# Optimization experiments

Hardware: AMD Instinct MI355X
Metric: run time of the kernel (lower is better)

Reference implementation:

```python
import jax, jax.numpy as jnp
import numpy as np

B, N, D, H, A = 1024, 16, 64, 64, 64
TAU = 0.01   # gumbel-softmax temperature from the source
EPS = 1e-10


def setup_inputs() -> dict:
    key = jax.random.key(0)
    ks = jax.random.split(key, 23)

    def rn(k, shape, s=0.05):
        return jax.random.normal(k, shape, dtype=jnp.float32) * s

    return {
        "obs": jax.random.normal(ks[0], (B, N, D), dtype=jnp.float32),
        "hidden_state": jax.random.normal(ks[1], (B * N, A), dtype=jnp.float32),
        "gumbel_u": jax.random.uniform(ks[2], (B * N * (N - 1), 2), dtype=jnp.float32,
                                       minval=1e-6, maxval=1.0 - 1e-6),
        "W_enc": rn(ks[3], (D, H)), "b_enc": rn(ks[4], (H,)),
        "Wih_f": rn(ks[5], (3 * H, 2 * H)), "Whh_f": rn(ks[6], (3 * H, H)),
        "bih_f": rn(ks[7], (3 * H,)), "bhh_f": rn(ks[8], (3 * H,)),
        "Wih_b": rn(ks[9], (3 * H, 2 * H)), "Whh_b": rn(ks[10], (3 * H, H)),
        "bih_b": rn(ks[11], (3 * H,)), "bhh_b": rn(ks[12], (3 * H,)),
        "W_hard": rn(ks[13], (2 * H, 2)), "b_hard": rn(ks[14], (2,)),
        "Wq": rn(ks[15], (H, A)), "Wk": rn(ks[16], (H, A)),
        "Wv": rn(ks[17], (H, A)), "b_v": rn(ks[18], (A,)),
        "Wih_c": rn(ks[19], (3 * A, A)), "Whh_c": rn(ks[20], (3 * A, A)),
        "bih_c": rn(ks[21], (3 * A,)), "bhh_c": rn(ks[22], (3 * A,)),
    }


def _gru_scan(x_seq, Wih, Whh, bih, bhh):
    # x_seq: [T, BN, 2H]; PyTorch GRU gate order r, z, n. Input projection
    # for all timesteps is precomputed (one big GEMM) outside the scan.
    gi = jnp.einsum('tbd,gd->tbg', x_seq, Wih) + bih  # [T, BN, 3H]
    h0 = jnp.zeros((x_seq.shape[1], Whh.shape[1]), x_seq.dtype)

    def step(h, gi_t):
        gh = h @ Whh.T + bhh
        i_r, i_z, i_n = jnp.split(gi_t, 3, axis=-1)
        h_r, h_z, h_n = jnp.split(gh, 3, axis=-1)
        r = jax.nn.sigmoid(i_r + h_r)
        z = jax.nn.sigmoid(i_z + h_z)
        n = jnp.tanh(i_n + r * h_n)
        h_new = (1.0 - z) * n + z * h
        return h_new, h_new

    _, out = jax.lax.scan(step, h0, gi)
    return out  # [T, BN, H]


def _gru_cell(x, h, Wih, Whh, bih, bhh):
    gi = x @ Wih.T + bih
    gh = h @ Whh.T + bhh
    i_r, i_z, i_n = jnp.split(gi, 3, axis=-1)
    h_r, h_z, h_n = jnp.split(gh, 3, axis=-1)
    r = jax.nn.sigmoid(i_r + h_r)
    z = jax.nn.sigmoid(i_z + h_z)
    n = jnp.tanh(i_n + r * h_n)
    return (1.0 - z) * n + z * h


def reference(obs, hidden_state, gumbel_u, W_enc, b_enc,
              Wih_f, Whh_f, bih_f, bhh_f, Wih_b, Whh_b, bih_b, bhh_b,
              W_hard, b_hard, Wq, Wk, Wv, b_v,
              Wih_c, Whh_c, bih_c, bhh_c):
    b, n, d = obs.shape
    h_enc = jax.nn.relu(obs @ W_enc + b_enc)          # [B, N, H]
    h_flat = h_enc.reshape(-1, H)                      # [B*N, H]

    # static neighbor index table: row i lists all j != i
    j_idx = np.array([[j for j in range(n) if j != i] for i in range(n)])  # [N, N-1]

    # pairwise concat features, vectorized (replaces the double python loop)
    h_j = h_enc[:, j_idx]                               # [B, N, N-1, H]
    h_i = jnp.broadcast_to(h_enc[:, :, None, :], h_j.shape)
    pair = jnp.concatenate([h_i, h_j], axis=-1)        # [B, N, N-1, 2H]
    input_hard = pair.transpose(2, 0, 1, 3).reshape(n - 1, b * n, 2 * H)

    # bidirectional GRU over the N-1 neighbor axis
    out_f = _gru_scan(input_hard, Wih_f, Whh_f, bih_f, bhh_f)
    out_b = _gru_scan(input_hard[::-1], Wih_b, Whh_b, bih_b, bhh_b)[::-1]
    h_hard = jnp.concatenate([out_f, out_b], axis=-1)  # [N-1, B*N, 2H]
    h_hard = h_hard.transpose(1, 0, 2).reshape(-1, 2 * H)

    # hard gate: gumbel-softmax (soft sample, tau=0.01), take channel 1
    logits = h_hard @ W_hard + b_hard                   # [B*N*(N-1), 2]
    g = -jnp.log(-jnp.log(gumbel_u + EPS) + EPS)
    hard = jax.nn.softmax((logits + g) / TAU, axis=-1)
    hard_w = hard[:, 1].reshape(b, n, n - 1)            # [B, N, N-1]

    # scaled dot-product attention over neighbors j != i
    q = (h_flat @ Wq).reshape(b, n, A)
    k = (h_flat @ Wk).reshape(b, n, A)
    v = jax.nn.relu(h_flat @ Wv + b_v).reshape(b, n, A)
    k_j = k[:, j_idx]                                   # [B, N, N-1, A]
    v_j = v[:, j_idx]
    score = jnp.einsum('bna,bnja->bnj', q, k_j) / float(np.sqrt(A))
    soft = jax.nn.softmax(score, axis=-1)
    x = jnp.einsum('bnja,bnj->bna', v_j, soft * hard_w).reshape(b * n, A)

    return _gru_cell(x, hidden_state, Wih_c, Whh_c, bih_c, bhh_c)
```

## Files before the change

### kernel.cpp

```cpp
#include <hip/hip_runtime.h>
#include <hip/hip_bf16.h>
#include <stdint.h>

#define NNODE 16384
#define TAU_ 0.01f
#define EPSG 1e-10f

#define OFF_WENC 0
#define OFF_BENC 4096
#define OFF_WIHF_H 4160
#define OFF_WIHF_L 16448
#define OFF_WHHF_H 28736
#define OFF_BIHF 41024
#define OFF_BHHF 41216
#define OFF_WIHB_H 41408
#define OFF_WIHB_L 53696
#define OFF_WHHB_H 65984
#define OFF_BIHB 78272
#define OFF_BHHB 78464
#define OFF_WHARD 78656
#define OFF_BHARD 78912
#define OFF_WQT_H 78914
#define OFF_WQT_L 80962
#define OFF_WKT_H 83010
#define OFF_WKT_L 85058
#define OFF_WVT_H 87106
#define OFF_WVT_L 89154
#define OFF_BV 91202
#define OFF_WIHC_H 91266
#define OFF_WIHC_L 97410
#define OFF_WHHC_H 103554
#define OFF_WHHC_L 109698
#define OFF_BIHC 115842
#define OFF_BHHC 116034
#define OFF_WENCT_H 118784
#define OFF_WENCT_L 120832
#define OFF_YF 131072
#define OFF_YB (OFF_YF + 491520)
#define WS_FLOATS (OFF_YB + 491520)

typedef float  v4f __attribute__((ext_vector_type(4)));
typedef short  v8s __attribute__((ext_vector_type(8)));

__device__ __forceinline__ float rcpf(float x){ return __builtin_amdgcn_rcpf(x); }
__device__ __forceinline__ float sigf(float x){ return rcpf(1.0f + __expf(-x)); }
__device__ __forceinline__ float tanhfast(float x){ return 1.0f - 2.0f*rcpf(__expf(2.0f*x)+1.0f); }
__device__ __forceinline__ unsigned short f2bf(float f){
  __hip_bfloat16 h = __float2bfloat16(f);
  return *reinterpret_cast<unsigned short*>(&h);
}
__device__ __forceinline__ float bf2f(unsigned short u){
  union { unsigned int i; float f; } v; v.i = ((unsigned int)u) << 16; return v.f;
}

struct Prep {
  const float* s[20];
  int n[20];
  int o[20];
};
__global__ void k_prep(Prep p, float* __restrict__ ws){
  int a = blockIdx.y;
  int i = blockIdx.x * blockDim.x + threadIdx.x;
  if (i < p.n[a]) ws[p.o[a] + i] = p.s[a][i];
}

__global__ void k_prep2(const float* __restrict__ wenc,
                        const float* __restrict__ wihf, const float* __restrict__ wihb,
                        const float* __restrict__ whhf, const float* __restrict__ whhb,
                        const float* __restrict__ wq,   const float* __restrict__ wk,
                        const float* __restrict__ wv,   const float* __restrict__ wihc,
                        const float* __restrict__ whhc,
                        float* __restrict__ ws){
  int a = blockIdx.y;
  int i = blockIdx.x * blockDim.x + threadIdx.x;
  if (a == 0 || (a >= 5 && a <= 7)){
    if (i < 4096){
      const float* src = (a==0) ? wenc : (a==5) ? wq : (a==6) ? wk : wv;
      int oh = (a==0) ? OFF_WENCT_H : (a==5) ? OFF_WQT_H : (a==6) ? OFF_WKT_H : OFF_WVT_H;
      int ol = (a==0) ? OFF_WENCT_L : oh + 2048;
      float x = src[((i & 63) << 6) | (i >> 6)];
      unsigned short h = f2bf(x);
      unsigned short l = f2bf(x - bf2f(h));
      ((unsigned short*)(ws + oh))[i] = h;
      ((unsigned short*)(ws + ol))[i] = l;
    }
  } else if (a == 1 || a == 2){
    if (i < 24576){
      float x = (a == 1 ? wihf : wihb)[i];
      unsigned short h = f2bf(x);
      unsigned short l = f2bf(x - bf2f(h));
      ((unsigned short*)(ws + (a == 1 ? OFF_WIHF_H : OFF_WIHB_H)))[i] = h;
      ((unsigned short*)(ws + (a == 1 ? OFF_WIHF_L : OFF_WIHB_L)))[i] = l;
    }
  } else if (a == 3 || a == 4){
    if (i < 12288){
      float x = (a == 3 ? whhf : whhb)[i];
      ((unsigned short*)(ws + (a == 3 ? OFF_WHHF_H : OFF_WHHB_H)))[i] = f2bf(x);
    }
  } else {
    if (i < 12288){
      float x = (a == 8 ? wihc : whhc)[i];
      unsigned short h = f2bf(x);
      unsigned short l = f2bf(x - bf2f(h));
      int oh = (a == 8 ? OFF_WIHC_H : OFF_WHHC_H);
      ((unsigned short*)(ws + oh))[i] = h;
      ((unsigned short*)(ws + oh + 6144))[i] = l;
    }
  }
}

__global__ __launch_bounds__(256, 2) void k_gru(const float* __restrict__ obs,
                                                float* __restrict__ ws){
  __shared__ float smem[9216];
  float* s_u2 = smem;
  unsigned short* s_obs_h = (unsigned short*)(smem + 6272);
  unsigned short* s_obs_l = s_obs_h + 2304;
  unsigned short* s_hbu   = (unsigned short*)(smem + 6272);
  float* s_red = smem + 9088;

  const int tid = threadIdx.x;
  const int nl  = tid & 63;
  const int grp = __builtin_amdgcn_readfirstlane(tid >> 6);
  const int dir = blockIdx.x >> 9;
  const int base = (blockIdx.x & 511) * 32;
  const int lw = grp >> 1;
  const int nw = grp & 1;
  const int q  = nl >> 4;
  const int i_c = nl & 15;
  const int node = 16*nw + i_c;

  {
    float4 a = *(const float4*)&obs[base*64 + tid*8];
    float4 b = *(const float4*)&obs[base*64 + tid*8 + 4];
    int nn = tid >> 3, d0 = (tid & 7)*8;
    union { v8s v; unsigned short u[8]; } H, L;
    float xs[8] = {a.x,a.y,a.z,a.w,b.x,b.y,b.z,b.w};
    #pragma unroll
    for (int e = 0; e < 8; e++){
      H.u[e] = f2bf(xs[e]);
      L.u[e] = f2bf(xs[e] - bf2f(H.u[e]));
    }
    *(v8s*)&s_obs_h[nn*72 + d0] = H.v;
    *(v8s*)&s_obs_l[nn*72 + d0] = L.v;
  }
  __syncthreads();

  const float* benc = ws + OFF_BENC;
  const unsigned short* wtH = (const unsigned short*)(ws + OFF_WENCT_H);
  const unsigned short* wtL = (const unsigned short*)(ws + OFF_WENCT_L);
  v4f dEnc[2];
  {
    v8s obH[2], obL[2];
    #pragma unroll
    for (int kc = 0; kc < 2; kc++){
      int ba = node*72 + kc*32 + q*8;
      obH[kc] = *(const v8s*)&s_obs_h[ba];
      obL[kc] = *(const v8s*)&s_obs_l[ba];
    }
    #pragma unroll
    for (int tt = 0; tt < 2; tt++){
      int lT = 2*lw + tt;
      float4 bi = *(const float4*)&benc[16*lT + 4*q];
      v4f d = (v4f){bi.x, bi.y, bi.z, bi.w};
      #pragma unroll
      for (int kc = 0; kc < 2; kc++){
        int aa = (16*lT + i_c)*64 + kc*32 + q*8;
        v8s aH = *(const v8s*)&wtH[aa];
        v8s aL = *(const v8s*)&wtL[aa];
        d = __builtin_amdgcn_mfma_f32_16x16x32_bf16(aH, obH[kc], d, 0,0,0);
        d = __builtin_amdgcn_mfma_f32_16x16x32_bf16(aH, obL[kc], d, 0,0,0);
        d = __builtin_amdgcn_mfma_f32_16x16x32_bf16(aL, obH[kc], d, 0,0,0);
      }
      dEnc[tt] = d;
    }
  }
  __syncthreads();
  #pragma unroll
  for (int tt = 0; tt < 2; tt++){
    int lT = 2*lw + tt;
    unsigned short hh[4], ll[4];
    #pragma unroll
    for (int r = 0; r < 4; r++){
      float v = fmaxf(dEnc[tt][r], 0.0f);
      hh[r] = f2bf(v);
      ll[r] = f2bf(v - bf2f(hh[r]));
    }
    int wa = node*72 + 16*lT + 4*q;
    *(uint2*)&s_obs_h[wa] = make_uint2((unsigned)hh[0] | ((unsigned)hh[1]<<16),
                                       (unsigned)hh[2] | ((unsigned)hh[3]<<16));
    *(uint2*)&s_obs_l[wa] = make_uint2((unsigned)ll[0] | ((unsigned)ll[1]<<16),
                                       (unsigned)ll[2] | ((unsigned)ll[3]<<16));
  }
  __syncthreads();

  const float* bih = ws + (dir ? OFF_BIHB : OFF_BIHF);
  const float* bhh = ws + (dir ? OFF_BHHB : OFF_BHHF);
  const unsigned short* wiH = (const unsigned short*)(ws + (dir ? OFF_WIHB_H : OFF_WIHF_H));
  const unsigned short* wiL = (const unsigned short*)(ws + (dir ? OFF_WIHB_L : OFF_WIHF_L));
  const unsigned short* whH = (const unsigned short*)(ws + (dir ? OFF_WHHB_H : OFF_WHHF_H));

  v8s hbH[2], hbL[2];
  #pragma unroll
  for (int kc = 0; kc < 2; kc++){
    int ba = node*72 + kc*32 + q*8;
    hbH[kc] = *(const v8s*)&s_obs_h[ba];
    hbL[kc] = *(const v8s*)&s_obs_l[ba];
  }

  #pragma unroll
  for (int m = 0; m < 6; m++){
    int T = 6*lw + m;
    v4f d = (v4f){0.f,0.f,0.f,0.f};
    #pragma unroll
    for (int kc = 0; kc < 2; kc++){
      int aa = (16*T + i_c)*128 + 64 + kc*32 + q*8;
      v8s aH = *(const v8s*)&wiH[aa];
      v8s aL = *(const v8s*)&wiL[aa];
      d = __builtin_amdgcn_mfma_f32_16x16x32_bf16(aH, hbH[kc], d, 0,0,0);
      d = __builtin_amdgcn_mfma_f32_16x16x32_bf16(aH, hbL[kc], d, 0,0,0);
      d = __builtin_amdgcn_mfma_f32_16x16x32_bf16(aL, hbH[kc], d, 0,0,0);
    }
    *(v4f*)&s_u2[node*196 + 16*T + 4*q] = d;
  }

  v4f cbr[2], cbz[2], cbn[2], bhn4[2];
  #pragma unroll
  for (int g = 0; g < 3; g++){
    #pragma unroll
    for (int t2 = 0; t2 < 2; t2++){
      int row0 = 64*g + 32*lw + 16*t2 + 4*q;
      float4 bi = *(const float4*)&bih[row0];
      v4f d;
      if (g < 2){
        float4 bh = *(const float4*)&bhh[row0];
        d = (v4f){bi.x+bh.x, bi.y+bh.y, bi.z+bh.z, bi.w+bh.w};
      } else {
        d = (v4f){bi.x, bi.y, bi.z, bi.w};
      }
      int T = (64*g + 32*lw + 16*t2) >> 4;
      #pragma unroll
      for (int kc = 0; kc < 2; kc++){
        int aa = (16*T + i_c)*128 + kc*32 + q*8;
        v8s aH = *(const v8s*)&wiH[aa];
        v8s aL = *(const v8s*)&wiL[aa];
        d = __builtin_amdgcn_mfma_f32_16x16x32_bf16(aH, hbH[kc], d, 0,0,0);
        d = __builtin_amdgcn_mfma_f32_16x16x32_bf16(aH, hbL[kc], d, 0,0,0);
        d = __builtin_amdgcn_mfma_f32_16x16x32_bf16(aL, hbH[kc], d, 0,0,0);
      }
      if (g == 0) cbr[t2] = d; else if (g == 1) cbz[t2] = d; else cbn[t2] = d;
    }
  }
  #pragma unroll
  for (int t2 = 0; t2 < 2; t2++){
    int row0 = 128 + 32*lw + 16*t2 + 4*q;
    float4 nh = *(const float4*)&bhh[row0];
    bhn4[t2] = (v4f){nh.x, nh.y, nh.z, nh.w};
  }

  v8s afr[2][2], afz[2][2], afn[2][2];
  #pragma unroll
  for (int t2 = 0; t2 < 2; t2++){
    #pragma unroll
    for (int kc = 0; kc < 2; kc++){
      #pragma unroll
      for (int g = 0; g < 3; g++){
        int row = g*64 + 32*lw + 16*t2 + i_c;
        v8s a = *(const v8s*)&whH[row*64 + kc*32 + q*8];
        if (g == 0) afr[t2][kc] = a; else if (g == 1) afz[t2][kc] = a; else afn[t2][kc] = a;
      }
    }
  }

  const float* whard = ws + OFF_WHARD + dir*128;
  float wh0[8], wh1[8];
  #pragma unroll
  for (int t2 = 0; t2 < 2; t2++){
    #pragma unroll
    for (int r = 0; r < 4; r++){
      int l = 32*lw + 16*t2 + 4*q + r;
      wh0[t2*4+r] = whard[l*2];
      wh1[t2*4+r] = whard[l*2+1];
    }
  }
  __syncthreads();

  float* yout = ws + (dir ? OFF_YB : OFF_YF);

  float hv[8];
  #pragma unroll
  for (int m = 0; m < 8; m++) hv[m] = 0.0f;

  for (int kk = 0; kk < 15; kk++){
    const int t  = dir ? (14 - kk) : kk;
    const int j  = t + (t >= i_c ? 1 : 0);
    const int jl = 16*nw + j;
    const int rb = kk & 1;
    const int wb = (kk + 1) & 1;

    v8s b0, b1;
    if (kk > 0){
      const unsigned short* rp = s_hbu + rb*2816 + node*88 + q*8;
      b0 = *(const v8s*)(rp);
      b1 = *(const v8s*)(rp + 32);
    }

    float a0p = 0.f, a1p = 0.f;
    #pragma unroll
    for (int t2 = 0; t2 < 2; t2++){
      int l0 = 32*lw + 16*t2 + 4*q;
      v4f dr = cbr[t2], dz = cbz[t2];
      v4f dn = (v4f){0.f,0.f,0.f,0.f};
      if (kk > 0){
        dr = __builtin_amdgcn_mfma_f32_16x16x32_bf16(afr[t2][0], b0, dr, 0,0,0);
        dr = __builtin_amdgcn_mfma_f32_16x16x32_bf16(afr[t2][1], b1, dr, 0,0,0);
        dz = __builtin_amdgcn_mfma_f32_16x16x32_bf16(afz[t2][0], b0, dz, 0,0,0);
        dz = __builtin_amdgcn_mfma_f32_16x16x32_bf16(afz[t2][1], b1, dz, 0,0,0);
        dn = __builtin_amdgcn_mfma_f32_16x16x32_bf16(afn[t2][0], b0, dn, 0,0,0);
        dn = __builtin_amdgcn_mfma_f32_16x16x32_bf16(afn[t2][1], b1, dn, 0,0,0);
      }
      v4f ur = *(const v4f*)&s_u2[jl*196 +       l0];
      v4f uz = *(const v4f*)&s_u2[jl*196 +  64 + l0];
      v4f un = *(const v4f*)&s_u2[jl*196 + 128 + l0];
      float hn[4];
      #pragma unroll
      for (int r = 0; r < 4; r++){
        float rg = sigf(dr[r] + ur[r]);
        float zg = sigf(dz[r] + uz[r]);
        float ng = tanhfast(cbn[t2][r] + un[r] + rg*(bhn4[t2][r] + dn[r]));
        float hnew = (1.0f - zg)*ng + zg*hv[t2*4+r];
        hv[t2*4+r] = hnew;
        hn[r] = hnew;
        a0p += hnew*wh0[t2*4+r];
        a1p += hnew*wh1[t2*4+r];
      }
      unsigned int p0 = (unsigned int)f2bf(hn[0]) | ((unsigned int)f2bf(hn[1]) << 16);
      unsigned int p1 = (unsigned int)f2bf(hn[2]) | ((unsigned int)f2bf(hn[3]) << 16);
      *(uint2*)(s_hbu + wb*2816 + node*88 + l0) = make_uint2(p0, p1);
    }

    a0p += __shfl_xor(a0p, 16); a0p += __shfl_xor(a0p, 32);
    a1p += __shfl_xor(a1p, 16); a1p += __shfl_xor(a1p, 32);
    float* sr = s_red + rb*64;
    if (lw == 0 && q == 0)
      *(float2*)&sr[node*2] = make_float2(a0p, a1p);
    __syncthreads();
    if (lw == 1 && q == 0){
      float2 pp = *(const float2*)&sr[node*2];
      *(float2*)&yout[((base + node)*15 + t)*2] = make_float2(a0p + pp.x, a1p + pp.y);
    }
  }
}

__global__ __launch_bounds__(256, 1) void k_attn(const float* __restrict__ obs,
                                                 const float* __restrict__ hid,
                                                 const float* __restrict__ gum,
                                                 float* __restrict__ ws,
                                                 float* __restrict__ out){
  __shared__ float smem[7200];
  unsigned short* s_obs_h = (unsigned short*)smem;
  unsigned short* s_obs_l = s_obs_h + 2304;
  float* s_q  = smem;
  unsigned short* s_h0h = (unsigned short*)smem;
  unsigned short* s_h0l = s_h0h + 2304;
  float* s_k  = smem + 2304;
  unsigned short* s_xh = (unsigned short*)(smem + 2304);
  unsigned short* s_xl = s_xh + 2304;
  float* s_v  = smem + 4608;
  float* s_co = smem + 6720;

  const int tid = threadIdx.x;
  const int nl  = tid & 63;
  const int grp = __builtin_amdgcn_readfirstlane(tid >> 6);
  const int base = blockIdx.x * 32;
  const int lw = grp >> 1;
  const int nw = grp & 1;
  const int q4 = nl >> 4;
  const int i_c = nl & 15;
  const int node = 16*nw + i_c;

  {
    float4 a = *(const float4*)&obs[base*64 + tid*8];
    float4 b = *(const float4*)&obs[base*64 + tid*8 + 4];
    int nn = tid >> 3, d0 = (tid & 7)*8;
    union { v8s v; unsigned short u[8]; } H, L;
    float xs[8] = {a.x,a.y,a.z,a.w,b.x,b.y,b.z,b.w};
    #pragma unroll
    for (int e = 0; e < 8; e++){
      H.u[e] = f2bf(xs[e]);
      L.u[e] = f2bf(xs[e] - bf2f(H.u[e]));
    }
    *(v8s*)&s_obs_h[nn*72 + d0] = H.v;
    *(v8s*)&s_obs_l[nn*72 + d0] = L.v;
  }
  __syncthreads();

  const float* benc = ws + OFF_BENC;
  const unsigned short* wtH = (const unsigned short*)(ws + OFF_WENCT_H);
  const unsigned short* wtL = (const unsigned short*)(ws + OFF_WENCT_L);
  v4f dEnc[2];
  {
    v8s obH[2], obL[2];
    #pragma unroll
    for (int kc = 0; kc < 2; kc++){
      int ba = node*72 + kc*32 + q4*8;
      obH[kc] = *(const v8s*)&s_obs_h[ba];
      obL[kc] = *(const v8s*)&s_obs_l[ba];
    }
    #pragma unroll
    for (int tt = 0; tt < 2; tt++){
      int lT = 2*lw + tt;
      float4 bi = *(const float4*)&benc[16*lT + 4*q4];
      v4f d = (v4f){bi.x, bi.y, bi.z, bi.w};
      #pragma unroll
      for (int kc = 0; kc < 2; kc++){
        int aa = (16*lT + i_c)*64 + kc*32 + q4*8;
        v8s aH = *(const v8s*)&wtH[aa];
        v8s aL = *(const v8s*)&wtL[aa];
        d = __builtin_amdgcn_mfma_f32_16x16x32_bf16(aH, obH[kc], d, 0,0,0);
        d = __builtin_amdgcn_mfma_f32_16x16x32_bf16(aH, obL[kc], d, 0,0,0);
        d = __builtin_amdgcn_mfma_f32_16x16x32_bf16(aL, obH[kc], d, 0,0,0);
      }
      dEnc[tt] = d;
    }
  }
  __syncthreads();
  #pragma unroll
  for (int tt = 0; tt < 2; tt++){
    int lT = 2*lw + tt;
    unsigned short hh[4], ll[4];
    #pragma unroll
    for (int r = 0; r < 4; r++){
      float v = fmaxf(dEnc[tt][r], 0.0f);
      hh[r] = f2bf(v);
      ll[r] = f2bf(v - bf2f(hh[r]));
    }
    int wa = node*72 + 16*lT + 4*q4;
    *(uint2*)&s_obs_h[wa] = make_uint2((unsigned)hh[0] | ((unsigned)hh[1]<<16),
                                       (unsigned)hh[2] | ((unsigned)hh[3]<<16));
    *(uint2*)&s_obs_l[wa] = make_uint2((unsigned)ll[0] | ((unsigned)ll[1]<<16),
                                       (unsigned)ll[2] | ((unsigned)ll[3]<<16));
  }
  __syncthreads();

  v8s hbH[2], hbL[2];
  #pragma unroll
  for (int kc = 0; kc < 2; kc++){
    int ba = node*72 + kc*32 + q4*8;
    hbH[kc] = *(const v8s*)&s_obs_h[ba];
    hbL[kc] = *(const v8s*)&s_obs_l[ba];
  }
  const unsigned short* wqH = (const unsigned short*)(ws + OFF_WQT_H);
  const unsigned short* wqL = (const unsigned short*)(ws + OFF_WQT_L);
  const unsigned short* wkH = (const unsigned short*)(ws + OFF_WKT_H);
  const unsigned short* wkL = (const unsigned short*)(ws + OFF_WKT_L);
  const unsigned short* wvH = (const unsigned short*)(ws + OFF_WVT_H);
  const unsigned short* wvL = (const unsigned short*)(ws + OFF_WVT_L);
  const float* bv = ws + OFF_BV;
  v4f dq[2], dk[2], dv[2];
  #pragma unroll
  for (int a2 = 0; a2 < 2; a2++){
    int aT = 2*lw + a2;
    v4f q_ = (v4f){0.f,0.f,0.f,0.f};
    v4f k_ = (v4f){0.f,0.f,0.f,0.f};
    float4 b4 = *(const float4*)&bv[16*aT + 4*q4];
    v4f v_ = (v4f){b4.x, b4.y, b4.z, b4.w};
    #pragma unroll
    for (int kc = 0; kc < 2; kc++){
      int ai = (16*aT + i_c)*64 + kc*32 + q4*8;
      v8s aH = *(const v8s*)&wqH[ai]; v8s aL = *(const v8s*)&wqL[ai];
      q_ = __builtin_amdgcn_mfma_f32_16x16x32_bf16(aH, hbH[kc], q_, 0,0,0);
      q_ = __builtin_amdgcn_mfma_f32_16x16x32_bf16(aH, hbL[kc], q_, 0,0,0);
      q_ = __builtin_amdgcn_mfma_f32_16x16x32_bf16(aL, hbH[kc], q_, 0,0,0);
      aH = *(const v8s*)&wkH[ai]; aL = *(const v8s*)&wkL[ai];
      k_ = __builtin_amdgcn_mfma_f32_16x16x32_bf16(aH, hbH[kc], k_, 0,0,0);
      k_ = __builtin_amdgcn_mfma_f32_16x16x32_bf16(aH, hbL[kc], k_, 0,0,0);
      k_ = __builtin_amdgcn_mfma_f32_16x16x32_bf16(aL, hbH[kc], k_, 0,0,0);
      aH = *(const v8s*)&wvH[ai]; aL = *(const v8s*)&wvL[ai];
      v_ = __builtin_amdgcn_mfma_f32_16x16x32_bf16(aH, hbH[kc], v_, 0,0,0);
      v_ = __builtin_amdgcn_mfma_f32_16x16x32_bf16(aH, hbL[kc], v_, 0,0,0);
      v_ = __builtin_amdgcn_mfma_f32_16x16x32_bf16(aL, hbH[kc], v_, 0,0,0);
    }
    dq[a2] = q_; dk[a2] = k_; dv[a2] = v_;
  }
  __syncthreads();

  #pragma unroll
  for (int a2 = 0; a2 < 2; a2++){
    int aT = 2*lw + a2;
    *(v4f*)&s_q[node*68 + 16*aT + 4*q4] = dq[a2];
    #pragma unroll
    for (int r = 0; r < 4; r++){
      s_k[(16*aT + 4*q4 + r)*33 + node] = dk[a2][r];
      s_v[(16*aT + 4*q4 + r)*33 + node] = fmaxf(dv[a2][r], 0.f);
    }
  }
  __syncthreads();

  const int n2  = tid >> 3;
  const int asl = tid & 7;
  const int ib2 = n2 & 15, jb2 = n2 & 16;
  float4 aq0 = *(const float4*)&s_q[n2*68 + asl*8];
  float4 aq1 = *(const float4*)&s_q[n2*68 + asl*8 + 4];
  float sc[15];
  #pragma unroll
  for (int t = 0; t < 15; t++){
    int jl = jb2 | (t + (t >= ib2 ? 1 : 0));
    const float* kp = s_k + (asl*8)*33 + jl;
    float s = aq0.x*kp[0]  + aq0.y*kp[33]  + aq0.z*kp[66]  + aq0.w*kp[99]
            + aq1.x*kp[132] + aq1.y*kp[165] + aq1.z*kp[198] + aq1.w*kp[231];
    s += __shfl_xor(s, 1); s += __shfl_xor(s, 2); s += __shfl_xor(s, 4);
    sc[t] = s * 0.125f;
  }
  {
    float m = sc[0];
    #pragma unroll
    for (int t = 1; t < 15; t++) m = fmaxf(m, sc[t]);
    float den = 0.f;
    #pragma unroll
    for (int t = 0; t < 15; t++) den += __expf(sc[t]-m);
    float rden = rcpf(den);
    const float bh0 = ws[OFF_BHARD], bh1 = ws[OFF_BHARD+1];
    const float* yF = ws + OFF_YF; const float* yB = ws + OFF_YB;
    #pragma unroll
    for (int t = 0; t < 15; t++){
      if ((t & 7) == asl){
        int rowb = ((base + n2)*15 + t)*2;
        float y0 = yF[rowb]   + yB[rowb]   + bh0;
        float y1 = yF[rowb+1] + yB[rowb+1] + bh1;
        float2 u2 = *(const float2*)&gum[rowb];
        float g0 = -__logf(-__logf(u2.x + EPSG) + EPSG);
        float g1 = -__logf(-__logf(u2.y + EPSG) + EPSG);
        float w  = sigf(((y1+g1) - (y0+g0)) * (1.0f/TAU_));
        s_co[t*32 + n2] = __expf(sc[t]-m)*rden*w;
      }
    }
  }
  __syncthreads();

  {
    float xa[8];
    #pragma unroll
    for (int il = 0; il < 8; il++) xa[il] = 0.f;
    #pragma unroll
    for (int t = 0; t < 15; t++){
      float c = s_co[t*32 + n2];
      int jl = jb2 | (t + (t >= ib2 ? 1 : 0));
      const float* vp = s_v + (asl*8)*33 + jl;
      xa[0] += c*vp[0];    xa[1] += c*vp[33];   xa[2] += c*vp[66];   xa[3] += c*vp[99];
      xa[4] += c*vp[132];  xa[5] += c*vp[165];  xa[6] += c*vp[198];  xa[7] += c*vp[231];
    }
    union { v8s v; unsigned short u[8]; } XH, XL;
    #pragma unroll
    for (int e = 0; e < 8; e++){
      XH.u[e] = f2bf(xa[e]);
      XL.u[e] = f2bf(xa[e] - bf2f(XH.u[e]));
    }
    *(v8s*)&s_xh[n2*72 + asl*8] = XH.v;
    *(v8s*)&s_xl[n2*72 + asl*8] = XL.v;
  }
  {
    float4 a = *(const float4*)&hid[base*64 + tid*8];
    float4 b = *(const float4*)&hid[base*64 + tid*8 + 4];
    int nn = tid >> 3, d0 = (tid & 7)*8;
    union { v8s v; unsigned short u[8]; } H, L;
    float xs[8] = {a.x,a.y,a.z,a.w,b.x,b.y,b.z,b.w};
    #pragma unroll
    for (int e = 0; e < 8; e++){
      H.u[e] = f2bf(xs[e]);
      L.u[e] = f2bf(xs[e] - bf2f(H.u[e]));
    }
    *(v8s*)&s_h0h[nn*72 + d0] = H.v;
    *(v8s*)&s_h0l[nn*72 + d0] = L.v;
  }
  __syncthreads();

  v8s xbH[2], xbL[2], h0H[2], h0L[2];
  #pragma unroll
  for (int kc = 0; kc < 2; kc++){
    int ba = node*72 + kc*32 + q4*8;
    xbH[kc] = *(const v8s*)&s_xh[ba];  xbL[kc] = *(const v8s*)&s_xl[ba];
    h0H[kc] = *(const v8s*)&s_h0h[ba]; h0L[kc] = *(const v8s*)&s_h0l[ba];
  }
  const unsigned short* wiH = (const unsigned short*)(ws + OFF_WIHC_H);
  const unsigned short* wiL = (const unsigned short*)(ws + OFF_WIHC_L);
  const unsigned short* whH = (const unsigned short*)(ws + OFF_WHHC_H);
  const unsigned short* whL = (const unsigned short*)(ws + OFF_WHHC_L);
  const float* bihc = ws + OFF_BIHC; const float* bhhc = ws + OFF_BHHC;
  v4f gi[3][2], gh[3][2];
  #pragma unroll
  for (int g = 0; g < 3; g++){
    #pragma unroll
    for (int u2 = 0; u2 < 2; u2++){
      int u = 2*lw + u2;
      int row0 = g*64 + 16*u + 4*q4;
      float4 bi = *(const float4*)&bihc[row0];
      float4 bh = *(const float4*)&bhhc[row0];
      v4f di, dh;
      if (g < 2){
        di = (v4f){bi.x+bh.x, bi.y+bh.y, bi.z+bh.z, bi.w+bh.w};
        dh = (v4f){0.f,0.f,0.f,0.f};
      } else {
        di = (v4f){bi.x, bi.y, bi.z, bi.w};
        dh = (v4f){bh.x, bh.y, bh.z, bh.w};
      }
      #pragma unroll
      for (int kc = 0; kc < 2; kc++){
        int ai = (g*64 + 16*u + i_c)*64 + kc*32 + q4*8;
        v8s aH = *(const v8s*)&wiH[ai]; v8s aL = *(const v8s*)&wiL[ai];
        di = __builtin_amdgcn_mfma_f32_16x16x32_bf16(aH, xbH[kc], di, 0,0,0);
        di = __builtin_amdgcn_mfma_f32_16x16x32_bf16(aH, xbL[kc], di, 0,0,0);
        di = __builtin_amdgcn_mfma_f32_16x16x32_bf16(aL, xbH[kc], di, 0,0,0);
        aH = *(const v8s*)&whH[ai]; aL = *(const v8s*)&whL[ai];
        dh = __builtin_amdgcn_mfma_f32_16x16x32_bf16(aH, h0H[kc], dh, 0,0,0);
        dh = __builtin_amdgcn_mfma_f32_16x16x32_bf16(aH, h0L[kc], dh, 0,0,0);
        dh = __builtin_amdgcn_mfma_f32_16x16x32_bf16(aL, h0H[kc], dh, 0,0,0);
      }
      gi[g][u2] = di; gh[g][u2] = dh;
    }
  }
  #pragma unroll
  for (int u2 = 0; u2 < 2; u2++){
    int l0 = 16*(2*lw + u2) + 4*q4;
    float4 h04 = *(const float4*)&hid[(base+node)*64 + l0];
    float hh[4] = {h04.x, h04.y, h04.z, h04.w};
    float ho[4];
    #pragma unroll
    for (int r = 0; r < 4; r++){
      float rg = sigf(gi[0][u2][r] + gh[0][u2][r]);
      float zg = sigf(gi[1][u2][r] + gh[1][u2][r]);
      float ng = tanhfast(gi[2][u2][r] + rg*gh[2][u2][r]);
      ho[r] = (1.0f - zg)*ng + zg*hh[r];
    }
    *(float4*)&out[(base+node)*64 + l0] = make_float4(ho[0], ho[1], ho[2], ho[3]);
  }
}

extern "C" void kernel_launch(void* const* d_in, const int* in_sizes, int n_in,
                              void* d_out, int out_size, void* d_ws, size_t ws_size,
                              hipStream_t stream){
  if (ws_size < (size_t)WS_FLOATS * sizeof(float)) return;
  float* ws = (float*)d_ws;
  static const int offs[20] = {OFF_WENC, OFF_BENC, 0, 0, OFF_BIHF, OFF_BHHF,
      0, 0, OFF_BIHB, OFF_BHHB, OFF_WHARD, OFF_BHARD, 0, 0, 0,
      OFF_BV, 0, 0, OFF_BIHC, OFF_BHHC};
  Prep p;
  for (int i = 0; i < 20; i++){
    p.s[i] = (const float*)d_in[3 + i];
    p.n[i] = in_sizes[3 + i];
    p.o[i] = offs[i];
  }
  p.n[2] = 0; p.n[3] = 0; p.n[6] = 0; p.n[7] = 0;
  p.n[12] = 0; p.n[13] = 0; p.n[14] = 0;
  p.n[16] = 0; p.n[17] = 0;
  hipLaunchKernelGGL(k_prep, dim3(96, 20), dim3(256), 0, stream, p, ws);
  hipLaunchKernelGGL(k_prep2, dim3(96, 10), dim3(256), 0, stream,
                     (const float*)d_in[3], (const float*)d_in[5], (const float*)d_in[9],
                     (const float*)d_in[6], (const float*)d_in[10],
                     (const float*)d_in[15], (const float*)d_in[16], (const float*)d_in[17],
                     (const float*)d_in[19], (const float*)d_in[20], ws);
  hipLaunchKernelGGL(k_gru,  dim3(1024),   dim3(256), 0, stream,
                     (const float*)d_in[0], ws);
  hipLaunchKernelGGL(k_attn, dim3(512),    dim3(256), 0, stream,
                     (const float*)d_in[0], (const float*)d_in[1],
                     (const float*)d_in[2], ws, (float*)d_out);
}
```

Before: 187.8 us.

## Fuse bidirectional GRU and attention kernels into one 512-thread block

Merges the separate GRU kernel and attention/output kernel into a single kernel with 512 threads per block, where both directions of the GRU run in the same block (waves split by direction). The encoder is computed once per block instead of three times, and the hard-gate logits stay in shared memory rather than going through a global workspace round-trip. This trades a larger shared-memory footprint and bigger blocks (possibly lower occupancy) and leaves half the threads idle during the attention phase.

```diff
diff --git a/kernel.cpp b/kernel.cpp
--- a/kernel.cpp
+++ b/kernel.cpp
@@ -109,83 +109,88 @@
   }
 }
 
-__global__ __launch_bounds__(256, 2) void k_gru(const float* __restrict__ obs,
-                                                float* __restrict__ ws){
-  __shared__ float smem[9216];
+__global__ __launch_bounds__(512, 2) void k_main(const float* __restrict__ obs,
+                                                 const float* __restrict__ hid,
+                                                 const float* __restrict__ gum,
+                                                 float* __restrict__ ws,
+                                                 float* __restrict__ out){
+  __shared__ float smem[20352];
   float* s_u2 = smem;
-  unsigned short* s_obs_h = (unsigned short*)(smem + 6272);
-  unsigned short* s_obs_l = s_obs_h + 2304;
-  unsigned short* s_hbu   = (unsigned short*)(smem + 6272);
-  float* s_red = smem + 9088;
+  unsigned short* s_B = (unsigned short*)(smem + 12544);
+  unsigned short* s_obs_h = s_B;
+  unsigned short* s_obs_l = s_B + 2304;
+  float* s_red = smem + 18176;
+  float* s_y   = smem + 18432;
+  float* s_q  = smem;
+  float* s_k  = smem + 2176;
+  float* s_v  = smem + 4288;
+  float* s_co = smem + 6400;
 
   const int tid = threadIdx.x;
   const int nl  = tid & 63;
   const int grp = __builtin_amdgcn_readfirstlane(tid >> 6);
-  const int dir = blockIdx.x >> 9;
-  const int base = (blockIdx.x & 511) * 32;
-  const int lw = grp >> 1;
-  const int nw = grp & 1;
-  const int q  = nl >> 4;
+  const int dir = grp >> 2;
+  const int sub = grp & 3;
+  const int lw  = sub >> 1;
+  const int nw  = grp & 1;
+  const int hi2 = grp >> 1;
+  const int q4  = nl >> 4;
   const int i_c = nl & 15;
   const int node = 16*nw + i_c;
-
-  {
-    float4 a = *(const float4*)&obs[base*64 + tid*8];
-    float4 b = *(const float4*)&obs[base*64 + tid*8 + 4];
-    int nn = tid >> 3, d0 = (tid & 7)*8;
-    union { v8s v; unsigned short u[8]; } H, L;
-    float xs[8] = {a.x,a.y,a.z,a.w,b.x,b.y,b.z,b.w};
-    #pragma unroll
-    for (int e = 0; e < 8; e++){
-      H.u[e] = f2bf(xs[e]);
-      L.u[e] = f2bf(xs[e] - bf2f(H.u[e]));
-    }
-    *(v8s*)&s_obs_h[nn*72 + d0] = H.v;
-    *(v8s*)&s_obs_l[nn*72 + d0] = L.v;
+  const int base = blockIdx.x * 32;
+
+  {
+    float4 a = *(const float4*)&obs[base*64 + tid*4];
+    int nn = tid >> 4, d0 = (tid & 15)*4;
+    unsigned short hh[4], ll[4];
+    float xs[4] = {a.x,a.y,a.z,a.w};
+    #pragma unroll
+    for (int e = 0; e < 4; e++){
+      hh[e] = f2bf(xs[e]);
+      ll[e] = f2bf(xs[e] - bf2f(hh[e]));
+    }
+    *(uint2*)&s_obs_h[nn*72 + d0] = make_uint2((unsigned)hh[0] | ((unsigned)hh[1]<<16),
+                                               (unsigned)hh[2] | ((unsigned)hh[3]<<16));
+    *(uint2*)&s_obs_l[nn*72 + d0] = make_uint2((unsigned)ll[0] | ((unsigned)ll[1]<<16),
+                                               (unsigned)ll[2] | ((unsigned)ll[3]<<16));
   }
   __syncthreads();
 
   const float* benc = ws + OFF_BENC;
   const unsigned short* wtH = (const unsigned short*)(ws + OFF_WENCT_H);
   const unsigned short* wtL = (const unsigned short*)(ws + OFF_WENCT_L);
-  v4f dEnc[2];
+  v4f dEnc;
   {
     v8s obH[2], obL[2];
     #pragma unroll
     for (int kc = 0; kc < 2; kc++){
-      int ba = node*72 + kc*32 + q*8;
+      int ba = node*72 + kc*32 + q4*8;
       obH[kc] = *(const v8s*)&s_obs_h[ba];
       obL[kc] = *(const v8s*)&s_obs_l[ba];
     }
-    #pragma unroll
-    for (int tt = 0; tt < 2; tt++){
-      int lT = 2*lw + tt;
-      float4 bi = *(const float4*)&benc[16*lT + 4*q];
-      v4f d = (v4f){bi.x, bi.y, bi.z, bi.w};
-      #pragma unroll
-      for (int kc = 0; kc < 2; kc++){
-        int aa = (16*lT + i_c)*64 + kc*32 + q*8;
-        v8s aH = *(const v8s*)&wtH[aa];
-        v8s aL = *(const v8s*)&wtL[aa];
-        d = __builtin_amdgcn_mfma_f32_16x16x32_bf16(aH, obH[kc], d, 0,0,0);
-        d = __builtin_amdgcn_mfma_f32_16x16x32_bf16(aH, obL[kc], d, 0,0,0);
-        d = __builtin_amdgcn_mfma_f32_16x16x32_bf16(aL, obH[kc], d, 0,0,0);
-      }
-      dEnc[tt] = d;
-    }
-  }
-  __syncthreads();
-  #pragma unroll
-  for (int tt = 0; tt < 2; tt++){
-    int lT = 2*lw + tt;
+    float4 bi = *(const float4*)&benc[16*hi2 + 4*q4];
+    v4f d = (v4f){bi.x, bi.y, bi.z, bi.w};
+    #pragma unroll
+    for (int kc = 0; kc < 2; kc++){
+      int aa = (16*hi2 + i_c)*64 + kc*32 + q4*8;
+      v8s aH = *(const v8s*)&wtH[aa];
+      v8s aL = *(const v8s*)&wtL[aa];
+      d = __builtin_amdgcn_mfma_f32_16x16x32_bf16(aH, obH[kc], d, 0,0,0);
+      d = __builtin_amdgcn_mfma_f32_16x16x32_bf16(aH, obL[kc], d, 0,0,0);
+      d = __builtin_amdgcn_mfma_f32_16x16x32_bf16(aL, obH[kc], d, 0,0,0);
+    }
+    dEnc = d;
+  }
+  __syncthreads();
+  {
     unsigned short hh[4], ll[4];
     #pragma unroll
     for (int r = 0; r < 4; r++){
-      float v = fmaxf(dEnc[tt][r], 0.0f);
+      float v = fmaxf(dEnc[r], 0.0f);
       hh[r] = f2bf(v);
       ll[r] = f2bf(v - bf2f(hh[r]));
     }
-    int wa = node*72 + 16*lT + 4*q;
+    int wa = node*72 + 16*hi2 + 4*q4;
     *(uint2*)&s_obs_h[wa] = make_uint2((unsigned)hh[0] | ((unsigned)hh[1]<<16),
                                        (unsigned)hh[2] | ((unsigned)hh[3]<<16));
     *(uint2*)&s_obs_l[wa] = make_uint2((unsigned)ll[0] | ((unsigned)ll[1]<<16),
@@ -193,255 +198,6 @@
   }
   __syncthreads();
 
-  const float* bih = ws + (dir ? OFF_BIHB : OFF_BIHF);
-  const float* bhh = ws + (dir ? OFF_BHHB : OFF_BHHF);
-  const unsigned short* wiH = (const unsigned short*)(ws + (dir ? OFF_WIHB_H : OFF_WIHF_H));
-  const unsigned short* wiL = (const unsigned short*)(ws + (dir ? OFF_WIHB_L : OFF_WIHF_L));
-  const unsigned short* whH = (const unsigned short*)(ws + (dir ? OFF_WHHB_H : OFF_WHHF_H));
-
-  v8s hbH[2], hbL[2];
-  #pragma unroll
-  for (int kc = 0; kc < 2; kc++){
-    int ba = node*72 + kc*32 + q*8;
-    hbH[kc] = *(const v8s*)&s_obs_h[ba];
-    hbL[kc] = *(const v8s*)&s_obs_l[ba];
-  }
-
-  #pragma unroll
-  for (int m = 0; m < 6; m++){
-    int T = 6*lw + m;
-    v4f d = (v4f){0.f,0.f,0.f,0.f};
-    #pragma unroll
-    for (int kc = 0; kc < 2; kc++){
-      int aa = (16*T + i_c)*128 + 64 + kc*32 + q*8;
-      v8s aH = *(const v8s*)&wiH[aa];
-      v8s aL = *(const v8s*)&wiL[aa];
-      d = __builtin_amdgcn_mfma_f32_16x16x32_bf16(aH, hbH[kc], d, 0,0,0);
-      d = __builtin_amdgcn_mfma_f32_16x16x32_bf16(aH, hbL[kc], d, 0,0,0);
-      d = __builtin_amdgcn_mfma_f32_16x16x32_bf16(aL, hbH[kc], d, 0,0,0);
-    }
-    *(v4f*)&s_u2[node*196 + 16*T + 4*q] = d;
-  }
-
-  v4f cbr[2], cbz[2], cbn[2], bhn4[2];
-  #pragma unroll
-  for (int g = 0; g < 3; g++){
-    #pragma unroll
-    for (int t2 = 0; t2 < 2; t2++){
-      int row0 = 64*g + 32*lw + 16*t2 + 4*q;
-      float4 bi = *(const float4*)&bih[row0];
-      v4f d;
-      if (g < 2){
-        float4 bh = *(const float4*)&bhh[row0];
-        d = (v4f){bi.x+bh.x, bi.y+bh.y, bi.z+bh.z, bi.w+bh.w};
-      } else {
-        d = (v4f){bi.x, bi.y, bi.z, bi.w};
-      }
-      int T = (64*g + 32*lw + 16*t2) >> 4;
-      #pragma unroll
-      for (int kc = 0; kc < 2; kc++){
-        int aa = (16*T + i_c)*128 + kc*32 + q*8;
-        v8s aH = *(const v8s*)&wiH[aa];
-        v8s aL = *(const v8s*)&wiL[aa];
-        d = __builtin_amdgcn_mfma_f32_16x16x32_bf16(aH, hbH[kc], d, 0,0,0);
-        d = __builtin_amdgcn_mfma_f32_16x16x32_bf16(aH, hbL[kc], d, 0,0,0);
-        d = __builtin_amdgcn_mfma_f32_16x16x32_bf16(aL, hbH[kc], d, 0,0,0);
-      }
-      if (g == 0) cbr[t2] = d; else if (g == 1) cbz[t2] = d; else cbn[t2] = d;
-    }
-  }
-  #pragma unroll
-  for (int t2 = 0; t2 < 2; t2++){
-    int row0 = 128 + 32*lw + 16*t2 + 4*q;
-    float4 nh = *(const float4*)&bhh[row0];
-    bhn4[t2] = (v4f){nh.x, nh.y, nh.z, nh.w};
-  }
-
-  v8s afr[2][2], afz[2][2], afn[2][2];
-  #pragma unroll
-  for (int t2 = 0; t2 < 2; t2++){
-    #pragma unroll
-    for (int kc = 0; kc < 2; kc++){
-      #pragma unroll
-      for (int g = 0; g < 3; g++){
-        int row = g*64 + 32*lw + 16*t2 + i_c;
-        v8s a = *(const v8s*)&whH[row*64 + kc*32 + q*8];
-        if (g == 0) afr[t2][kc] = a; else if (g == 1) afz[t2][kc] = a; else afn[t2][kc] = a;
-      }
-    }
-  }
-
-  const float* whard = ws + OFF_WHARD + dir*128;
-  float wh0[8], wh1[8];
-  #pragma unroll
-  for (int t2 = 0; t2 < 2; t2++){
-    #pragma unroll
-    for (int r = 0; r < 4; r++){
-      int l = 32*lw + 16*t2 + 4*q + r;
-      wh0[t2*4+r] = whard[l*2];
-      wh1[t2*4+r] = whard[l*2+1];
-    }
-  }
-  __syncthreads();
-
-  float* yout = ws + (dir ? OFF_YB : OFF_YF);
-
-  float hv[8];
-  #pragma unroll
-  for (int m = 0; m < 8; m++) hv[m] = 0.0f;
-
-  for (int kk = 0; kk < 15; kk++){
-    const int t  = dir ? (14 - kk) : kk;
-    const int j  = t + (t >= i_c ? 1 : 0);
-    const int jl = 16*nw + j;
-    const int rb = kk & 1;
-    const int wb = (kk + 1) & 1;
-
-    v8s b0, b1;
-    if (kk > 0){
-      const unsigned short* rp = s_hbu + rb*2816 + node*88 + q*8;
-      b0 = *(const v8s*)(rp);
-      b1 = *(const v8s*)(rp + 32);
-    }
-
-    float a0p = 0.f, a1p = 0.f;
-    #pragma unroll
-    for (int t2 = 0; t2 < 2; t2++){
-      int l0 = 32*lw + 16*t2 + 4*q;
-      v4f dr = cbr[t2], dz = cbz[t2];
-      v4f dn = (v4f){0.f,0.f,0.f,0.f};
-      if (kk > 0){
-        dr = __builtin_amdgcn_mfma_f32_16x16x32_bf16(afr[t2][0], b0, dr, 0,0,0);
-        dr = __builtin_amdgcn_mfma_f32_16x16x32_bf16(afr[t2][1], b1, dr, 0,0,0);
-        dz = __builtin_amdgcn_mfma_f32_16x16x32_bf16(afz[t2][0], b0, dz, 0,0,0);
-        dz = __builtin_amdgcn_mfma_f32_16x16x32_bf16(afz[t2][1], b1, dz, 0,0,0);
-        dn = __builtin_amdgcn_mfma_f32_16x16x32_bf16(afn[t2][0], b0, dn, 0,0,0);
-        dn = __builtin_amdgcn_mfma_f32_16x16x32_bf16(afn[t2][1], b1, dn, 0,0,0);
-      }
-      v4f ur = *(const v4f*)&s_u2[jl*196 +       l0];
-      v4f uz = *(const v4f*)&s_u2[jl*196 +  64 + l0];
-      v4f un = *(const v4f*)&s_u2[jl*196 + 128 + l0];
-      float hn[4];
-      #pragma unroll
-      for (int r = 0; r < 4; r++){
-        float rg = sigf(dr[r] + ur[r]);
-        float zg = sigf(dz[r] + uz[r]);
-        float ng = tanhfast(cbn[t2][r] + un[r] + rg*(bhn4[t2][r] + dn[r]));
-        float hnew = (1.0f - zg)*ng + zg*hv[t2*4+r];
-        hv[t2*4+r] = hnew;
-        hn[r] = hnew;
-        a0p += hnew*wh0[t2*4+r];
-        a1p += hnew*wh1[t2*4+r];
-      }
-      unsigned int p0 = (unsigned int)f2bf(hn[0]) | ((unsigned int)f2bf(hn[1]) << 16);
-      unsigned int p1 = (unsigned int)f2bf(hn[2]) | ((unsigned int)f2bf(hn[3]) << 16);
-      *(uint2*)(s_hbu + wb*2816 + node*88 + l0) = make_uint2(p0, p1);
-    }
-
-    a0p += __shfl_xor(a0p, 16); a0p += __shfl_xor(a0p, 32);
-    a1p += __shfl_xor(a1p, 16); a1p += __shfl_xor(a1p, 32);
-    float* sr = s_red + rb*64;
-    if (lw == 0 && q == 0)
-      *(float2*)&sr[node*2] = make_float2(a0p, a1p);
-    __syncthreads();
-    if (lw == 1 && q == 0){
-      float2 pp = *(const float2*)&sr[node*2];
-      *(float2*)&yout[((base + node)*15 + t)*2] = make_float2(a0p + pp.x, a1p + pp.y);
-    }
-  }
-}
-
-__global__ __launch_bounds__(256, 1) void k_attn(const float* __restrict__ obs,
-                                                 const float* __restrict__ hid,
-                                                 const float* __restrict__ gum,
-                                                 float* __restrict__ ws,
-                                                 float* __restrict__ out){
-  __shared__ float smem[7200];
-  unsigned short* s_obs_h = (unsigned short*)smem;
-  unsigned short* s_obs_l = s_obs_h + 2304;
-  float* s_q  = smem;
-  unsigned short* s_h0h = (unsigned short*)smem;
-  unsigned short* s_h0l = s_h0h + 2304;
-  float* s_k  = smem + 2304;
-  unsigned short* s_xh = (unsigned short*)(smem + 2304);
-  unsigned short* s_xl = s_xh + 2304;
-  float* s_v  = smem + 4608;
-  float* s_co = smem + 6720;
-
-  const int tid = threadIdx.x;
-  const int nl  = tid & 63;
-  const int grp = __builtin_amdgcn_readfirstlane(tid >> 6);
-  const int base = blockIdx.x * 32;
-  const int lw = grp >> 1;
-  const int nw = grp & 1;
-  const int q4 = nl >> 4;
-  const int i_c = nl & 15;
-  const int node = 16*nw + i_c;
-
-  {
-    float4 a = *(const float4*)&obs[base*64 + tid*8];
-    float4 b = *(const float4*)&obs[base*64 + tid*8 + 4];
-    int nn = tid >> 3, d0 = (tid & 7)*8;
-    union { v8s v; unsigned short u[8]; } H, L;
-    float xs[8] = {a.x,a.y,a.z,a.w,b.x,b.y,b.z,b.w};
-    #pragma unroll
-    for (int e = 0; e < 8; e++){
-      H.u[e] = f2bf(xs[e]);
-      L.u[e] = f2bf(xs[e] - bf2f(H.u[e]));
-    }
-    *(v8s*)&s_obs_h[nn*72 + d0] = H.v;
-    *(v8s*)&s_obs_l[nn*72 + d0] = L.v;
-  }
-  __syncthreads();
-
-  const float* benc = ws + OFF_BENC;
-  const unsigned short* wtH = (const unsigned short*)(ws + OFF_WENCT_H);
-  const unsigned short* wtL = (const unsigned short*)(ws + OFF_WENCT_L);
-  v4f dEnc[2];
-  {
-    v8s obH[2], obL[2];
-    #pragma unroll
-    for (int kc = 0; kc < 2; kc++){
-      int ba = node*72 + kc*32 + q4*8;
-      obH[kc] = *(const v8s*)&s_obs_h[ba];
-      obL[kc] = *(const v8s*)&s_obs_l[ba];
-    }
-    #pragma unroll
-    for (int tt = 0; tt < 2; tt++){
-      int lT = 2*lw + tt;
-      float4 bi = *(const float4*)&benc[16*lT + 4*q4];
-      v4f d = (v4f){bi.x, bi.y, bi.z, bi.w};
-      #pragma unroll
-      for (int kc = 0; kc < 2; kc++){
-        int aa = (16*lT + i_c)*64 + kc*32 + q4*8;
-        v8s aH = *(const v8s*)&wtH[aa];
-        v8s aL = *(const v8s*)&wtL[aa];
-        d = __builtin_amdgcn_mfma_f32_16x16x32_bf16(aH, obH[kc], d, 0,0,0);
-        d = __builtin_amdgcn_mfma_f32_16x16x32_bf16(aH, obL[kc], d, 0,0,0);
-        d = __builtin_amdgcn_mfma_f32_16x16x32_bf16(aL, obH[kc], d, 0,0,0);
-      }
-      dEnc[tt] = d;
-    }
-  }
-  __syncthreads();
-  #pragma unroll
-  for (int tt = 0; tt < 2; tt++){
-    int lT = 2*lw + tt;
-    unsigned short hh[4], ll[4];
-    #pragma unroll
-    for (int r = 0; r < 4; r++){
-      float v = fmaxf(dEnc[tt][r], 0.0f);
-      hh[r] = f2bf(v);
-      ll[r] = f2bf(v - bf2f(hh[r]));
-    }
-    int wa = node*72 + 16*lT + 4*q4;
-    *(uint2*)&s_obs_h[wa] = make_uint2((unsigned)hh[0] | ((unsigned)hh[1]<<16),
-                                       (unsigned)hh[2] | ((unsigned)hh[3]<<16));
-    *(uint2*)&s_obs_l[wa] = make_uint2((unsigned)ll[0] | ((unsigned)ll[1]<<16),
-                                       (unsigned)ll[2] | ((unsigned)ll[3]<<16));
-  }
-  __syncthreads();
-
   v8s hbH[2], hbL[2];
   #pragma unroll
   for (int kc = 0; kc < 2; kc++){
@@ -449,24 +205,23 @@
     hbH[kc] = *(const v8s*)&s_obs_h[ba];
     hbL[kc] = *(const v8s*)&s_obs_l[ba];
   }
-  const unsigned short* wqH = (const unsigned short*)(ws + OFF_WQT_H);
-  const unsigned short* wqL = (const unsigned short*)(ws + OFF_WQT_L);
-  const unsigned short* wkH = (const unsigned short*)(ws + OFF_WKT_H);
-  const unsigned short* wkL = (const unsigned short*)(ws + OFF_WKT_L);
-  const unsigned short* wvH = (const unsigned short*)(ws + OFF_WVT_H);
-  const unsigned short* wvL = (const unsigned short*)(ws + OFF_WVT_L);
-  const float* bv = ws + OFF_BV;
-  v4f dq[2], dk[2], dv[2];
-  #pragma unroll
-  for (int a2 = 0; a2 < 2; a2++){
-    int aT = 2*lw + a2;
+
+  v4f dq, dk, dv;
+  {
+    const unsigned short* wqH = (const unsigned short*)(ws + OFF_WQT_H);
+    const unsigned short* wqL = (const unsigned short*)(ws + OFF_WQT_L);
+    const unsigned short* wkH = (const unsigned short*)(ws + OFF_WKT_H);
+    const unsigned short* wkL = (const unsigned short*)(ws + OFF_WKT_L);
+    const unsigned short* wvH = (const unsigned short*)(ws + OFF_WVT_H);
+    const unsigned short* wvL = (const unsigned short*)(ws + OFF_WVT_L);
+    const float* bv = ws + OFF_BV;
     v4f q_ = (v4f){0.f,0.f,0.f,0.f};
     v4f k_ = (v4f){0.f,0.f,0.f,0.f};
-    float4 b4 = *(const float4*)&bv[16*aT + 4*q4];
+    float4 b4 = *(const float4*)&bv[16*hi2 + 4*q4];
     v4f v_ = (v4f){b4.x, b4.y, b4.z, b4.w};
     #pragma unroll
     for (int kc = 0; kc < 2; kc++){
-      int ai = (16*aT + i_c)*64 + kc*32 + q4*8;
+      int ai = (16*hi2 + i_c)*64 + kc*32 + q4*8;
       v8s aH = *(const v8s*)&wqH[ai]; v8s aL = *(const v8s*)&wqL[ai];
       q_ = __builtin_amdgcn_mfma_f32_16x16x32_bf16(aH, hbH[kc], q_, 0,0,0);
       q_ = __builtin_amdgcn_mfma_f32_16x16x32_bf16(aH, hbL[kc], q_, 0,0,0);
@@ -480,18 +235,165 @@
       v_ = __builtin_amdgcn_mfma_f32_16x16x32_bf16(aH, hbL[kc], v_, 0,0,0);
       v_ = __builtin_amdgcn_mfma_f32_16x16x32_bf16(aL, hbH[kc], v_, 0,0,0);
     }
-    dq[a2] = q_; dk[a2] = k_; dv[a2] = v_;
-  }
-  __syncthreads();
-
-  #pragma unroll
-  for (int a2 = 0; a2 < 2; a2++){
-    int aT = 2*lw + a2;
-    *(v4f*)&s_q[node*68 + 16*aT + 4*q4] = dq[a2];
+    dq = q_; dk = k_; dv = v_;
+  }
+
+  const float* bih = ws + (dir ? OFF_BIHB : OFF_BIHF);
+  const float* bhh = ws + (dir ? OFF_BHHB : OFF_BHHF);
+  const unsigned short* wiH = (const unsigned short*)(ws + (dir ? OFF_WIHB_H : OFF_WIHF_H));
+  const unsigned short* wiL = (const unsigned short*)(ws + (dir ? OFF_WIHB_L : OFF_WIHF_L));
+  const unsigned short* whH = (const unsigned short*)(ws + (dir ? OFF_WHHB_H : OFF_WHHF_H));
+  float* myu2 = s_u2 + dir*6272;
+
+  #pragma unroll
+  for (int m = 0; m < 6; m++){
+    int T = 6*lw + m;
+    v4f d = (v4f){0.f,0.f,0.f,0.f};
+    #pragma unroll
+    for (int kc = 0; kc < 2; kc++){
+      int aa = (16*T + i_c)*128 + 64 + kc*32 + q4*8;
+      v8s aH = *(const v8s*)&wiH[aa];
+      v8s aL = *(const v8s*)&wiL[aa];
+      d = __builtin_amdgcn_mfma_f32_16x16x32_bf16(aH, hbH[kc], d, 0,0,0);
+      d = __builtin_amdgcn_mfma_f32_16x16x32_bf16(aH, hbL[kc], d, 0,0,0);
+      d = __builtin_amdgcn_mfma_f32_16x16x32_bf16(aL, hbH[kc], d, 0,0,0);
+    }
+    *(v4f*)&myu2[node*196 + 16*T + 4*q4] = d;
+  }
+
+  v4f cbr[2], cbz[2], cbn[2], bhn4[2];
+  #pragma unroll
+  for (int g = 0; g < 3; g++){
+    #pragma unroll
+    for (int t2 = 0; t2 < 2; t2++){
+      int row0 = 64*g + 32*lw + 16*t2 + 4*q4;
+      float4 bi = *(const float4*)&bih[row0];
+      v4f d;
+      if (g < 2){
+        float4 bh = *(const float4*)&bhh[row0];
+        d = (v4f){bi.x+bh.x, bi.y+bh.y, bi.z+bh.z, bi.w+bh.w};
+      } else {
+        d = (v4f){bi.x, bi.y, bi.z, bi.w};
+      }
+      int T = (64*g + 32*lw + 16*t2) >> 4;
+      #pragma unroll
+      for (int kc = 0; kc < 2; kc++){
+        int aa = (16*T + i_c)*128 + kc*32 + q4*8;
+        v8s aH = *(const v8s*)&wiH[aa];
+        v8s aL = *(const v8s*)&wiL[aa];
+        d = __builtin_amdgcn_mfma_f32_16x16x32_bf16(aH, hbH[kc], d, 0,0,0);
+        d = __builtin_amdgcn_mfma_f32_16x16x32_bf16(aH, hbL[kc], d, 0,0,0);
+        d = __builtin_amdgcn_mfma_f32_16x16x32_bf16(aL, hbH[kc], d, 0,0,0);
+      }
+      if (g == 0) cbr[t2] = d; else if (g == 1) cbz[t2] = d; else cbn[t2] = d;
+    }
+  }
+  #pragma unroll
+  for (int t2 = 0; t2 < 2; t2++){
+    int row0 = 128 + 32*lw + 16*t2 + 4*q4;
+    float4 nh = *(const float4*)&bhh[row0];
+    bhn4[t2] = (v4f){nh.x, nh.y, nh.z, nh.w};
+  }
+
+  v8s afr[2][2], afz[2][2], afn[2][2];
+  #pragma unroll
+  for (int t2 = 0; t2 < 2; t2++){
+    #pragma unroll
+    for (int kc = 0; kc < 2; kc++){
+      #pragma unroll
+      for (int g = 0; g < 3; g++){
+        int row = g*64 + 32*lw + 16*t2 + i_c;
+        v8s a = *(const v8s*)&whH[row*64 + kc*32 + q4*8];
+        if (g == 0) afr[t2][kc] = a; else if (g == 1) afz[t2][kc] = a; else afn[t2][kc] = a;
+      }
+    }
+  }
+
+  const float* whard = ws + OFF_WHARD + dir*128;
+  float wh0[8], wh1[8];
+  #pragma unroll
+  for (int t2 = 0; t2 < 2; t2++){
     #pragma unroll
     for (int r = 0; r < 4; r++){
-      s_k[(16*aT + 4*q4 + r)*33 + node] = dk[a2][r];
-      s_v[(16*aT + 4*q4 + r)*33 + node] = fmaxf(dv[a2][r], 0.f);
+      int l = 32*lw + 16*t2 + 4*q4 + r;
+      wh0[t2*4+r] = whard[l*2];
+      wh1[t2*4+r] = whard[l*2+1];
+    }
+  }
+  __syncthreads();
+
+  unsigned short* myh = s_B + dir*5632;
+  float hv[8];
+  #pragma unroll
+  for (int m = 0; m < 8; m++) hv[m] = 0.0f;
+
+  for (int kk = 0; kk < 15; kk++){
+    const int t  = dir ? (14 - kk) : kk;
+    const int j  = t + (t >= i_c ? 1 : 0);
+    const int jl = 16*nw + j;
+    const int rb = kk & 1;
+    const int wb = (kk + 1) & 1;
+
+    v8s b0, b1;
+    if (kk > 0){
+      const unsigned short* rp = myh + rb*2816 + node*88 + q4*8;
+      b0 = *(const v8s*)(rp);
+      b1 = *(const v8s*)(rp + 32);
+    }
+
+    float a0p = 0.f, a1p = 0.f;
+    #pragma unroll
+    for (int t2 = 0; t2 < 2; t2++){
+      int l0 = 32*lw + 16*t2 + 4*q4;
+      v4f dr = cbr[t2], dz = cbz[t2];
+      v4f dn = (v4f){0.f,0.f,0.f,0.f};
+      if (kk > 0){
+        dr = __builtin_amdgcn_mfma_f32_16x16x32_bf16(afr[t2][0], b0, dr, 0,0,0);
+        dr = __builtin_amdgcn_mfma_f32_16x16x32_bf16(afr[t2][1], b1, dr, 0,0,0);
+        dz = __builtin_amdgcn_mfma_f32_16x16x32_bf16(afz[t2][0], b0, dz, 0,0,0);
+        dz = __builtin_amdgcn_mfma_f32_16x16x32_bf16(afz[t2][1], b1, dz, 0,0,0);
+        dn = __builtin_amdgcn_mfma_f32_16x16x32_bf16(afn[t2][0], b0, dn, 0,0,0);
+        dn = __builtin_amdgcn_mfma_f32_16x16x32_bf16(afn[t2][1], b1, dn, 0,0,0);
+      }
+      v4f ur = *(const v4f*)&myu2[jl*196 +       l0];
+      v4f uz = *(const v4f*)&myu2[jl*196 +  64 + l0];
+      v4f un = *(const v4f*)&myu2[jl*196 + 128 + l0];
+      float hn[4];
+      #pragma unroll
+      for (int r = 0; r < 4; r++){
+        float rg = sigf(dr[r] + ur[r]);
+        float zg = sigf(dz[r] + uz[r]);
+        float ng = tanhfast(cbn[t2][r] + un[r] + rg*(bhn4[t2][r] + dn[r]));
+        float hnew = (1.0f - zg)*ng + zg*hv[t2*4+r];
+        hv[t2*4+r] = hnew;
+        hn[r] = hnew;
+        a0p += hnew*wh0[t2*4+r];
+        a1p += hnew*wh1[t2*4+r];
+      }
+      unsigned int p0 = (unsigned int)f2bf(hn[0]) | ((unsigned int)f2bf(hn[1]) << 16);
+      unsigned int p1 = (unsigned int)f2bf(hn[2]) | ((unsigned int)f2bf(hn[3]) << 16);
+      *(uint2*)(myh + wb*2816 + node*88 + l0) = make_uint2(p0, p1);
+    }
+
+    a0p += __shfl_xor(a0p, 16); a0p += __shfl_xor(a0p, 32);
+    a1p += __shfl_xor(a1p, 16); a1p += __shfl_xor(a1p, 32);
+    float* sr = s_red + dir*128 + rb*64;
+    if (lw == 0 && q4 == 0)
+      *(float2*)&sr[node*2] = make_float2(a0p, a1p);
+    __syncthreads();
+    if (lw == 1 && q4 == 0){
+      float2 pp = *(const float2*)&sr[node*2];
+      *(float2*)&s_y[dir*960 + (node*15 + t)*2] = make_float2(a0p + pp.x, a1p + pp.y);
+    }
+  }
+  __syncthreads();
+
+  {
+    *(v4f*)&s_q[node*68 + 16*hi2 + 4*q4] = dq;
+    #pragma unroll
+    for (int r = 0; r < 4; r++){
+      s_k[(16*hi2 + 4*q4 + r)*33 + node] = dk[r];
+      s_v[(16*hi2 + 4*q4 + r)*33 + node] = fmaxf(dv[r], 0.f);
     }
   }
   __syncthreads();
@@ -499,19 +401,19 @@
   const int n2  = tid >> 3;
   const int asl = tid & 7;
   const int ib2 = n2 & 15, jb2 = n2 & 16;
-  float4 aq0 = *(const float4*)&s_q[n2*68 + asl*8];
-  float4 aq1 = *(const float4*)&s_q[n2*68 + asl*8 + 4];
-  float sc[15];
-  #pragma unroll
-  for (int t = 0; t < 15; t++){
-    int jl = jb2 | (t + (t >= ib2 ? 1 : 0));
-    const float* kp = s_k + (asl*8)*33 + jl;
-    float s = aq0.x*kp[0]  + aq0.y*kp[33]  + aq0.z*kp[66]  + aq0.w*kp[99]
-            + aq1.x*kp[132] + aq1.y*kp[165] + aq1.z*kp[198] + aq1.w*kp[231];
-    s += __shfl_xor(s, 1); s += __shfl_xor(s, 2); s += __shfl_xor(s, 4);
-    sc[t] = s * 0.125f;
-  }
-  {
+  if (tid < 256){
+    float4 aq0 = *(const float4*)&s_q[n2*68 + asl*8];
+    float4 aq1 = *(const float4*)&s_q[n2*68 + asl*8 + 4];
+    float sc[15];
+    #pragma unroll
+    for (int t = 0; t < 15; t++){
+      int jl = jb2 | (t + (t >= ib2 ? 1 : 0));
+      const float* kp = s_k + (asl*8)*33 + jl;
+      float s = aq0.x*kp[0]   + aq0.y*kp[33]  + aq0.z*kp[66]  + aq0.w*kp[99]
+              + aq1.x*kp[132] + aq1.y*kp[165] + aq1.z*kp[198] + aq1.w*kp[231];
+      s += __shfl_xor(s, 1); s += __shfl_xor(s, 2); s += __shfl_xor(s, 4);
+      sc[t] = s * 0.125f;
+    }
     float m = sc[0];
     #pragma unroll
     for (int t = 1; t < 15; t++) m = fmaxf(m, sc[t]);
@@ -520,14 +422,13 @@
     for (int t = 0; t < 15; t++) den += __expf(sc[t]-m);
     float rden = rcpf(den);
     const float bh0 = ws[OFF_BHARD], bh1 = ws[OFF_BHARD+1];
-    const float* yF = ws + OFF_YF; const float* yB = ws + OFF_YB;
     #pragma unroll
     for (int t = 0; t < 15; t++){
       if ((t & 7) == asl){
-        int rowb = ((base + n2)*15 + t)*2;
-        float y0 = yF[rowb]   + yB[rowb]   + bh0;
-        float y1 = yF[rowb+1] + yB[rowb+1] + bh1;
-        float2 u2 = *(const float2*)&gum[rowb];
+        int yi = (n2*15 + t)*2;
+        float y0 = s_y[yi]     + s_y[960 + yi]     + bh0;
+        float y1 = s_y[yi + 1] + s_y[960 + yi + 1] + bh1;
+        float2 u2 = *(const float2*)&gum[((base + n2)*15 + t)*2];
         float g0 = -__logf(-__logf(u2.x + EPSG) + EPSG);
         float g1 = -__logf(-__logf(u2.y + EPSG) + EPSG);
         float w  = sigf(((y1+g1) - (y0+g0)) * (1.0f/TAU_));
@@ -537,7 +438,11 @@
   }
   __syncthreads();
 
-  {
+  unsigned short* s_xh  = s_B;
+  unsigned short* s_xl  = s_B + 2304;
+  unsigned short* s_h0h = s_B + 4608;
+  unsigned short* s_h0l = s_B + 6912;
+  if (tid < 256){
     float xa[8];
     #pragma unroll
     for (int il = 0; il < 8; il++) xa[il] = 0.f;
@@ -559,40 +464,39 @@
     *(v8s*)&s_xl[n2*72 + asl*8] = XL.v;
   }
   {
-    float4 a = *(const float4*)&hid[base*64 + tid*8];
-    float4 b = *(const float4*)&hid[base*64 + tid*8 + 4];
-    int nn = tid >> 3, d0 = (tid & 7)*8;
-    union { v8s v; unsigned short u[8]; } H, L;
-    float xs[8] = {a.x,a.y,a.z,a.w,b.x,b.y,b.z,b.w};
-    #pragma unroll
-    for (int e = 0; e < 8; e++){
-      H.u[e] = f2bf(xs[e]);
-      L.u[e] = f2bf(xs[e] - bf2f(H.u[e]));
-    }
-    *(v8s*)&s_h0h[nn*72 + d0] = H.v;
-    *(v8s*)&s_h0l[nn*72 + d0] = L.v;
-  }
-  __syncthreads();
-
-  v8s xbH[2], xbL[2], h0H[2], h0L[2];
-  #pragma unroll
-  for (int kc = 0; kc < 2; kc++){
-    int ba = node*72 + kc*32 + q4*8;
-    xbH[kc] = *(const v8s*)&s_xh[ba];  xbL[kc] = *(const v8s*)&s_xl[ba];
-    h0H[kc] = *(const v8s*)&s_h0h[ba]; h0L[kc] = *(const v8s*)&s_h0l[ba];
-  }
-  const unsigned short* wiH = (const unsigned short*)(ws + OFF_WIHC_H);
-  const unsigned short* wiL = (const unsigned short*)(ws + OFF_WIHC_L);
-  const unsigned short* whH = (const unsigned short*)(ws + OFF_WHHC_H);
-  const unsigned short* whL = (const unsigned short*)(ws + OFF_WHHC_L);
-  const float* bihc = ws + OFF_BIHC; const float* bhhc = ws + OFF_BHHC;
-  v4f gi[3][2], gh[3][2];
-  #pragma unroll
-  for (int g = 0; g < 3; g++){
-    #pragma unroll
-    for (int u2 = 0; u2 < 2; u2++){
-      int u = 2*lw + u2;
-      int row0 = g*64 + 16*u + 4*q4;
+    float4 a = *(const float4*)&hid[base*64 + tid*4];
+    int nn = tid >> 4, d0 = (tid & 15)*4;
+    unsigned short hh[4], ll[4];
+    float xs[4] = {a.x,a.y,a.z,a.w};
+    #pragma unroll
+    for (int e = 0; e < 4; e++){
+      hh[e] = f2bf(xs[e]);
+      ll[e] = f2bf(xs[e] - bf2f(hh[e]));
+    }
+    *(uint2*)&s_h0h[nn*72 + d0] = make_uint2((unsigned)hh[0] | ((unsigned)hh[1]<<16),
+                                             (unsigned)hh[2] | ((unsigned)hh[3]<<16));
+    *(uint2*)&s_h0l[nn*72 + d0] = make_uint2((unsigned)ll[0] | ((unsigned)ll[1]<<16),
+                                             (unsigned)ll[2] | ((unsigned)ll[3]<<16));
+  }
+  __syncthreads();
+
+  {
+    v8s xbH[2], xbL[2], h0H[2], h0L[2];
+    #pragma unroll
+    for (int kc = 0; kc < 2; kc++){
+      int ba = node*72 + kc*32 + q4*8;
+      xbH[kc] = *(const v8s*)&s_xh[ba];  xbL[kc] = *(const v8s*)&s_xl[ba];
+      h0H[kc] = *(const v8s*)&s_h0h[ba]; h0L[kc] = *(const v8s*)&s_h0l[ba];
+    }
+    const unsigned short* wiH2 = (const unsigned short*)(ws + OFF_WIHC_H);
+    const unsigned short* wiL2 = (const unsigned short*)(ws + OFF_WIHC_L);
+    const unsigned short* whH2 = (const unsigned short*)(ws + OFF_WHHC_H);
+    const unsigned short* whL2 = (const unsigned short*)(ws + OFF_WHHC_L);
+    const float* bihc = ws + OFF_BIHC; const float* bhhc = ws + OFF_BHHC;
+    v4f gi[3], gh[3];
+    #pragma unroll
+    for (int g = 0; g < 3; g++){
+      int row0 = g*64 + 16*hi2 + 4*q4;
       float4 bi = *(const float4*)&bihc[row0];
       float4 bh = *(const float4*)&bhhc[row0];
       v4f di, dh;
@@ -605,31 +509,28 @@
       }
       #pragma unroll
       for (int kc = 0; kc < 2; kc++){
-        int ai = (g*64 + 16*u + i_c)*64 + kc*32 + q4*8;
-        v8s aH = *(const v8s*)&wiH[ai]; v8s aL = *(const v8s*)&wiL[ai];
+        int ai = (g*64 + 16*hi2 + i_c)*64 + kc*32 + q4*8;
+        v8s aH = *(const v8s*)&wiH2[ai]; v8s aL = *(const v8s*)&wiL2[ai];
         di = __builtin_amdgcn_mfma_f32_16x16x32_bf16(aH, xbH[kc], di, 0,0,0);
         di = __builtin_amdgcn_mfma_f32_16x16x32_bf16(aH, xbL[kc], di, 0,0,0);
         di = __builtin_amdgcn_mfma_f32_16x16x32_bf16(aL, xbH[kc], di, 0,0,0);
-        aH = *(const v8s*)&whH[ai]; aL = *(const v8s*)&whL[ai];
+        aH = *(const v8s*)&whH2[ai]; aL = *(const v8s*)&whL2[ai];
         dh = __builtin_amdgcn_mfma_f32_16x16x32_bf16(aH, h0H[kc], dh, 0,0,0);
         dh = __builtin_amdgcn_mfma_f32_16x16x32_bf16(aH, h0L[kc], dh, 0,0,0);
         dh = __builtin_amdgcn_mfma_f32_16x16x32_bf16(aL, h0H[kc], dh, 0,0,0);
       }
-      gi[g][u2] = di; gh[g][u2] = dh;
-    }
-  }
-  #pragma unroll
-  for (int u2 = 0; u2 < 2; u2++){
-    int l0 = 16*(2*lw + u2) + 4*q4;
+      gi[g] = di; gh[g] = dh;
+    }
+    int l0 = 16*hi2 + 4*q4;
     float4 h04 = *(const float4*)&hid[(base+node)*64 + l0];
-    float hh[4] = {h04.x, h04.y, h04.z, h04.w};
+    float hh4[4] = {h04.x, h04.y, h04.z, h04.w};
     float ho[4];
     #pragma unroll
     for (int r = 0; r < 4; r++){
-      float rg = sigf(gi[0][u2][r] + gh[0][u2][r]);
-      float zg = sigf(gi[1][u2][r] + gh[1][u2][r]);
-      float ng = tanhfast(gi[2][u2][r] + rg*gh[2][u2][r]);
-      ho[r] = (1.0f - zg)*ng + zg*hh[r];
+      float rg = sigf(gi[0][r] + gh[0][r]);
+      float zg = sigf(gi[1][r] + gh[1][r]);
+      float ng = tanhfast(gi[2][r] + rg*gh[2][r]);
+      ho[r] = (1.0f - zg)*ng + zg*hh4[r];
     }
     *(float4*)&out[(base+node)*64 + l0] = make_float4(ho[0], ho[1], ho[2], ho[3]);
   }
@@ -658,9 +559,7 @@
                      (const float*)d_in[6], (const float*)d_in[10],
                      (const float*)d_in[15], (const float*)d_in[16], (const float*)d_in[17],
                      (const float*)d_in[19], (const float*)d_in[20], ws);
-  hipLaunchKernelGGL(k_gru,  dim3(1024),   dim3(256), 0, stream,
-                     (const float*)d_in[0], ws);
-  hipLaunchKernelGGL(k_attn, dim3(512),    dim3(256), 0, stream,
+  hipLaunchKernelGGL(k_main, dim3(512), dim3(512), 0, stream,
                      (const float*)d_in[0], (const float*)d_in[1],
                      (const float*)d_in[2], ws, (float*)d_out);
 }
```

Result: slower. 203.2 us (+8.2%).
